# Kernel tuning notes

Hardware: AMD Instinct MI355X
Metric: run time of the kernel (lower is better)

## Reference

```python
import jax, jax.numpy as jnp
import numpy as np

EPS = 1e-6

def setup_inputs() -> dict:
    key = jax.random.key(0)
    ks = jax.random.split(key, 6)
    N, E, Din, H, D = 50000, 800000, 256, 4, 32
    x = jax.random.normal(ks[0], (N, Din), dtype=jnp.float32)
    adj_indices = jax.random.randint(ks[1], (E, 2), 0, N, dtype=jnp.int32)
    adj_weights = jax.random.uniform(ks[2], (E,), dtype=jnp.float32)
    W = jax.random.normal(ks[3], (Din, H * D), dtype=jnp.float32) * (1.0 / np.sqrt(Din))
    a_src = jax.random.normal(ks[4], (H, D), dtype=jnp.float32)
    a_dst = jax.random.normal(ks[5], (H, D), dtype=jnp.float32)
    return {"x": x, "adj_indices": adj_indices, "adj_weights": adj_weights,
            "W": W, "a_src": a_src, "a_dst": a_dst}

def reference(x, adj_indices, adj_weights, W, a_src, a_dst):
    N = x.shape[0]
    H, D = a_src.shape
    h = (x @ W).reshape(N, H, D)                       # [N,H,D]
    src = adj_indices[:, 0]
    dst = adj_indices[:, 1]
    hs = h[src]                                        # [E,H,D]
    hd = h[dst]                                        # [E,H,D]
    raw = jnp.einsum('ehd,hd->eh', hs, a_src) + jnp.einsum('ehd,hd->eh', hd, a_dst)
    gate = jnp.clip(adj_weights, EPS, None)[:, None]   # [E,1]
    scores = jnp.tanh(raw) + jnp.log(gate)             # [E,H]
    # per-destination segment softmax (numerically stable)
    seg_max = jax.ops.segment_max(scores, dst, num_segments=N)   # [N,H]
    ex = jnp.exp(scores - seg_max[dst])
    denom = jax.ops.segment_sum(ex, dst, num_segments=N)         # [N,H]
    alpha = ex / denom[dst]                            # softmax over edges per dst
    alpha = alpha * gate
    messages = alpha[:, :, None] * hs                  # [E,H,D]
    out = jax.ops.segment_sum(messages, dst, num_segments=N)     # [N,H,D]
    out = out.reshape(N, H * D)
    return jax.nn.gelu(out, approximate=False)
```

## Files before the change

### kernel.cpp

```cpp
#include <hip/hip_runtime.h>
#include <hip/hip_bf16.h>

#define N_NODES 50000
#define N_EDGES 800000
#define DIN 256
#define HD 128
#define NH 4
#define CAP 64
#define CSTR 16

#define GROWS 64
#define LDKH 136

#define GEMM_BLOCKS ((N_NODES + GROWS - 1) / GROWS)
#define SCAT_BLOCKS ((N_EDGES + 255) / 256)

typedef __bf16 bf16x8 __attribute__((ext_vector_type(8)));
typedef float  f32x4  __attribute__((ext_vector_type(4)));

static __device__ __forceinline__ unsigned short f2bu(float v) {
  union { __hip_bfloat16 b; unsigned short u; } c;
  c.b = __float2bfloat16(v);
  return c.u;
}

static __device__ __forceinline__ unsigned short f2hu(float v) {
  union { _Float16 h; unsigned short u; } c;
  c.h = (_Float16)v;
  return c.u;
}

static __device__ __forceinline__ float hu2f(unsigned short u) {
  union { _Float16 h; unsigned short u; } c;
  c.u = u;
  return (float)c.h;
}

__global__ void init_kernel(const float* __restrict__ W,
                            unsigned short* __restrict__ Wt,
                            int* __restrict__ cursor) {
  int i = blockIdx.x * 256 + threadIdx.x;
  if (i < HD * DIN) {
    int c = i >> 8, k = i & 255;
    Wt[c * 256 + k] = f2bu(W[k * HD + c]);
  }
  if (i < N_NODES * CSTR) cursor[i] = 0;
}

__global__ __launch_bounds__(256, 4) void fused_gemm_scatter(
    const float* __restrict__ x,
    const unsigned short* __restrict__ Wt,
    const float* __restrict__ a_src,
    const float* __restrict__ a_dst,
    unsigned short* __restrict__ hbf,
    float* __restrict__ ssrc,
    float* __restrict__ sdst,
    const int2* __restrict__ adj,
    const float* __restrict__ wts,
    int* __restrict__ cursor,
    unsigned int* __restrict__ slots) {
  __shared__ unsigned short xs[GROWS * LDKH];
  const int tid = threadIdx.x;

  if (blockIdx.x >= GEMM_BLOCKS) {
    int e = (blockIdx.x - GEMM_BLOCKS) * 256 + tid;
    if (e >= N_EDGES) return;
    int2 sd = adj[e];
    if ((unsigned)sd.x >= (unsigned)N_NODES || (unsigned)sd.y >= (unsigned)N_NODES) return;
    float g = fmaxf(wts[e], 1e-6f);
    int pos = atomicAdd(&cursor[sd.y * CSTR], 1);
    if (pos >= CAP) pos = CAP - 1;
    unsigned packed = ((unsigned)f2hu(g) << 16) | (unsigned)sd.x;
    __builtin_nontemporal_store(packed, &slots[((size_t)sd.y << 6) + pos]);
    return;
  }

  const int row0 = blockIdx.x * GROWS;
  const int wid  = tid >> 6;
  const int lane = tid & 63;
  const int m    = lane & 15;
  const int q    = lane >> 4;

  f32x4 acc[8];
#pragma unroll
  for (int t = 0; t < 8; t++) acc[t] = (f32x4){0.f, 0.f, 0.f, 0.f};

#pragma unroll
  for (int ks = 0; ks < 2; ks++) {
#pragma unroll
    for (int it = 0; it < 8; it++) {
      int i  = it * 256 + tid;
      int r  = i >> 5;
      int kq = i & 31;
      int row = row0 + r;
      float4 v = make_float4(0.f, 0.f, 0.f, 0.f);
      if (row < N_NODES) v = *(const float4*)(x + (size_t)row * DIN + ks * 128 + 4 * kq);
      ushort4 b;
      b.x = f2bu(v.x); b.y = f2bu(v.y); b.z = f2bu(v.z); b.w = f2bu(v.w);
      *(ushort4*)&xs[r * LDKH + 4 * kq] = b;
    }
    __syncthreads();

    const unsigned short* xbase = &xs[(wid * 16 + m) * LDKH];
#pragma unroll
    for (int s = 0; s < 4; s++) {
      bf16x8 afrag = *(const bf16x8*)(xbase + 32 * s + 8 * q);
#pragma unroll
      for (int t = 0; t < 8; t++) {
        bf16x8 bfrag = *(const bf16x8*)(Wt + (size_t)(16 * t + m) * 256 + ks * 128 + 32 * s + 8 * q);
        acc[t] = __builtin_amdgcn_mfma_f32_16x16x32_bf16(afrag, bfrag, acc[t], 0, 0, 0);
      }
    }
    __syncthreads();
  }

#pragma unroll
  for (int t = 0; t < 8; t++) {
#pragma unroll
    for (int r = 0; r < 4; r++) {
      int row = row0 + wid * 16 + q * 4 + r;
      if (row < N_NODES) hbf[(size_t)row * HD + 16 * t + m] = f2bu(acc[t][r]);
    }
  }

  float as[8], ad[8];
#pragma unroll
  for (int t = 0; t < 8; t++) {
    as[t] = a_src[16 * t + m];
    ad[t] = a_dst[16 * t + m];
  }
#pragma unroll
  for (int r = 0; r < 4; r++) {
    float ps[NH] = {0.f, 0.f, 0.f, 0.f};
    float pd[NH] = {0.f, 0.f, 0.f, 0.f};
#pragma unroll
    for (int t = 0; t < 8; t++) {
      ps[t >> 1] = fmaf(acc[t][r], as[t], ps[t >> 1]);
      pd[t >> 1] = fmaf(acc[t][r], ad[t], pd[t >> 1]);
    }
#pragma unroll
    for (int mm = 8; mm >= 1; mm >>= 1) {
#pragma unroll
      for (int hh = 0; hh < NH; hh++) {
        ps[hh] += __shfl_xor(ps[hh], mm, 64);
        pd[hh] += __shfl_xor(pd[hh], mm, 64);
      }
    }
    int row = row0 + wid * 16 + q * 4 + r;
    if (m == 0 && row < N_NODES) {
#pragma unroll
      for (int hh = 0; hh < NH; hh++) {
        ssrc[row * NH + hh] = ps[hh];
        sdst[row * NH + hh] = pd[hh];
      }
    }
  }
}

__global__ __launch_bounds__(128, 8) void node_kernel(
    const int* __restrict__ cursor,
    const unsigned int* __restrict__ slots,
    const float4* __restrict__ ssrc4,
    const float4* __restrict__ sdst4,
    const unsigned int* __restrict__ hbf32,
    float* __restrict__ out) {
  const int tid  = threadIdx.x;
  const int wid  = tid >> 6;
  const int lane = tid & 63;
  const int n    = blockIdx.x * 2 + wid;
  const int hh   = lane >> 4;

  int deg = cursor[n * CSTR];
  if (deg > CAP) deg = CAP;

  __shared__ int    sidx[2][CAP];
  __shared__ float4 swv[2][CAP];

  float4 ex = make_float4(0.f, 0.f, 0.f, 0.f);
  if (lane < deg) {
    unsigned sl = slots[((size_t)n << 6) + lane];
    int s = (int)(sl & 0xffffu);
    float g = hu2f((unsigned short)(sl >> 16));
    float4 ss = ssrc4[s];
    float4 sd = sdst4[n];
    ex.x = g * expf(tanhf(ss.x + sd.x));
    ex.y = g * expf(tanhf(ss.y + sd.y));
    ex.z = g * expf(tanhf(ss.z + sd.z));
    ex.w = g * expf(tanhf(ss.w + sd.w));
    sidx[wid][lane] = s;
    swv[wid][lane] = make_float4(ex.x * g, ex.y * g, ex.z * g, ex.w * g);
  }

  float4 tot = ex;
#pragma unroll
  for (int mm = 32; mm >= 1; mm >>= 1) {
    tot.x += __shfl_xor(tot.x, mm, 64);
    tot.y += __shfl_xor(tot.y, mm, 64);
    tot.z += __shfl_xor(tot.z, mm, 64);
    tot.w += __shfl_xor(tot.w, mm, 64);
  }
  float dn  = (hh == 0) ? tot.x : (hh == 1) ? tot.y : (hh == 2) ? tot.z : tot.w;
  float inv = (dn > 0.f) ? 1.f / dn : 0.f;
  __syncthreads();

  float acc0 = 0.f, acc1 = 0.f;
  int j = 0;
  for (; j + 4 <= deg; j += 4) {
    int s0 = sidx[wid][j + 0], s1 = sidx[wid][j + 1];
    int s2 = sidx[wid][j + 2], s3 = sidx[wid][j + 3];
    unsigned u0 = hbf32[(size_t)s0 * (HD / 2) + lane];
    unsigned u1 = hbf32[(size_t)s1 * (HD / 2) + lane];
    unsigned u2 = hbf32[(size_t)s2 * (HD / 2) + lane];
    unsigned u3 = hbf32[(size_t)s3 * (HD / 2) + lane];
    float w0 = ((const float*)&swv[wid][j + 0])[hh];
    float w1 = ((const float*)&swv[wid][j + 1])[hh];
    float w2 = ((const float*)&swv[wid][j + 2])[hh];
    float w3 = ((const float*)&swv[wid][j + 3])[hh];
    acc0 = fmaf(w0, __uint_as_float(u0 << 16), acc0);
    acc1 = fmaf(w0, __uint_as_float(u0 & 0xffff0000u), acc1);
    acc0 = fmaf(w1, __uint_as_float(u1 << 16), acc0);
    acc1 = fmaf(w1, __uint_as_float(u1 & 0xffff0000u), acc1);
    acc0 = fmaf(w2, __uint_as_float(u2 << 16), acc0);
    acc1 = fmaf(w2, __uint_as_float(u2 & 0xffff0000u), acc1);
    acc0 = fmaf(w3, __uint_as_float(u3 << 16), acc0);
    acc1 = fmaf(w3, __uint_as_float(u3 & 0xffff0000u), acc1);
  }
  for (; j < deg; j++) {
    int s0 = sidx[wid][j];
    unsigned u0 = hbf32[(size_t)s0 * (HD / 2) + lane];
    float w0 = ((const float*)&swv[wid][j])[hh];
    acc0 = fmaf(w0, __uint_as_float(u0 << 16), acc0);
    acc1 = fmaf(w0, __uint_as_float(u0 & 0xffff0000u), acc1);
  }
  acc0 *= inv;
  acc1 *= inv;

  float2 gl;
  gl.x = 0.5f * acc0 * (1.f + erff(acc0 * 0.70710678118654752f));
  gl.y = 0.5f * acc1 * (1.f + erff(acc1 * 0.70710678118654752f));
  *(float2*)&out[(size_t)n * HD + 2 * lane] = gl;
}

extern "C" void kernel_launch(void* const* d_in, const int* in_sizes, int n_in,
                              void* d_out, int out_size, void* d_ws, size_t ws_size,
                              hipStream_t stream) {
  const float* x     = (const float*)d_in[0];
  const int2*  adj   = (const int2*)d_in[1];
  const float* wts   = (const float*)d_in[2];
  const float* W     = (const float*)d_in[3];
  const float* a_src = (const float*)d_in[4];
  const float* a_dst = (const float*)d_in[5];
  float* out = (float*)d_out;

  char* p = (char*)d_ws;
  auto carve = [&](size_t bytes) {
    char* q = p;
    p += (bytes + 255) & ~(size_t)255;
    return (void*)q;
  };
  unsigned short* hbf = (unsigned short*)carve((size_t)N_NODES * HD * sizeof(unsigned short));
  unsigned short* Wt  = (unsigned short*)carve((size_t)HD * DIN * sizeof(unsigned short));
  float* ssrc   = (float*)carve((size_t)N_NODES * NH * sizeof(float));
  float* sdst   = (float*)carve((size_t)N_NODES * NH * sizeof(float));
  unsigned int* slots = (unsigned int*)carve((size_t)N_NODES * CAP * sizeof(unsigned int));
  int*   cursor = (int*)carve((size_t)N_NODES * CSTR * sizeof(int));

  init_kernel<<<(N_NODES * CSTR + 255) / 256, 256, 0, stream>>>(W, Wt, cursor);
  fused_gemm_scatter<<<GEMM_BLOCKS + SCAT_BLOCKS, 256, 0, stream>>>(
      x, Wt, a_src, a_dst, hbf, ssrc, sdst, adj, wts, cursor, slots);
  node_kernel<<<N_NODES / 2, 128, 0, stream>>>(cursor, slots, (const float4*)ssrc,
                                               (const float4*)sdst,
                                               (const unsigned int*)hbf, out);
}
```

Baseline: 192.6 us.

## Prefetch second K-half of x, pre-swizzle W fragments, unroll gather loop by eight

The GEMM stage now loads the second 128-column half of x into registers while the MFMAs for the first half run, so global latency overlaps with compute. W is pre-permuted in the init kernel into MFMA fragment order, making each B-fragment load one contiguous 16-byte read per lane. The node kernel's gather loop is unrolled from 4 to 8 edges to keep more independent loads in flight, and the launch bounds are relaxed on both kernels. The cost is higher register use, which may lower occupancy. The source index is also masked to 16 bits, which truncates node IDs above 65535 even though N is 50000.

```diff
diff --git a/kernel.cpp b/kernel.cpp
--- a/kernel.cpp
+++ b/kernel.cpp
@@ -37,19 +37,26 @@
 }
 
 __global__ void init_kernel(const float* __restrict__ W,
-                            unsigned short* __restrict__ Wt,
+                            unsigned short* __restrict__ WtF,
                             int* __restrict__ cursor) {
   int i = blockIdx.x * 256 + threadIdx.x;
   if (i < HD * DIN) {
-    int c = i >> 8, k = i & 255;
-    Wt[c * 256 + k] = f2bu(W[k * HD + c]);
+    int j    = i & 7;
+    int lane = (i >> 3) & 63;
+    int t    = (i >> 9) & 7;
+    int s    = (i >> 12) & 3;
+    int ks   = (i >> 14) & 1;
+    int m = lane & 15, q = lane >> 4;
+    int k = ks * 128 + 32 * s + 8 * q + j;
+    int c = 16 * t + m;
+    WtF[i] = f2bu(W[k * HD + c]);
   }
   if (i < N_NODES * CSTR) cursor[i] = 0;
 }
 
-__global__ __launch_bounds__(256, 4) void fused_gemm_scatter(
+__global__ void fused_gemm_scatter(
     const float* __restrict__ x,
-    const unsigned short* __restrict__ Wt,
+    const unsigned short* __restrict__ WtF,
     const float* __restrict__ a_src,
     const float* __restrict__ a_dst,
     unsigned short* __restrict__ hbf,
@@ -70,7 +77,7 @@
     float g = fmaxf(wts[e], 1e-6f);
     int pos = atomicAdd(&cursor[sd.y * CSTR], 1);
     if (pos >= CAP) pos = CAP - 1;
-    unsigned packed = ((unsigned)f2hu(g) << 16) | (unsigned)sd.x;
+    unsigned packed = ((unsigned)f2hu(g) << 16) | (unsigned)(sd.x & 0xffff);
     __builtin_nontemporal_store(packed, &slots[((size_t)sd.y << 6) + pos]);
     return;
   }
@@ -81,37 +88,76 @@
   const int m    = lane & 15;
   const int q    = lane >> 4;
 
+  float4 v0[8];
+#pragma unroll
+  for (int it = 0; it < 8; it++) {
+    int i = it * 256 + tid, r = i >> 5, kq = i & 31;
+    int row = row0 + r;
+    v0[it] = (row < N_NODES) ? *(const float4*)(x + (size_t)row * DIN + 4 * kq)
+                             : make_float4(0.f, 0.f, 0.f, 0.f);
+  }
+#pragma unroll
+  for (int it = 0; it < 8; it++) {
+    int i = it * 256 + tid, r = i >> 5, kq = i & 31;
+    ushort4 b;
+    b.x = f2bu(v0[it].x); b.y = f2bu(v0[it].y); b.z = f2bu(v0[it].z); b.w = f2bu(v0[it].w);
+    *(ushort4*)&xs[r * LDKH + 4 * kq] = b;
+  }
+  __syncthreads();
+
   f32x4 acc[8];
 #pragma unroll
   for (int t = 0; t < 8; t++) acc[t] = (f32x4){0.f, 0.f, 0.f, 0.f};
 
-#pragma unroll
-  for (int ks = 0; ks < 2; ks++) {
-#pragma unroll
-    for (int it = 0; it < 8; it++) {
-      int i  = it * 256 + tid;
-      int r  = i >> 5;
-      int kq = i & 31;
-      int row = row0 + r;
-      float4 v = make_float4(0.f, 0.f, 0.f, 0.f);
-      if (row < N_NODES) v = *(const float4*)(x + (size_t)row * DIN + ks * 128 + 4 * kq);
-      ushort4 b;
-      b.x = f2bu(v.x); b.y = f2bu(v.y); b.z = f2bu(v.z); b.w = f2bu(v.w);
-      *(ushort4*)&xs[r * LDKH + 4 * kq] = b;
-    }
-    __syncthreads();
-
-    const unsigned short* xbase = &xs[(wid * 16 + m) * LDKH];
-#pragma unroll
-    for (int s = 0; s < 4; s++) {
-      bf16x8 afrag = *(const bf16x8*)(xbase + 32 * s + 8 * q);
-#pragma unroll
-      for (int t = 0; t < 8; t++) {
-        bf16x8 bfrag = *(const bf16x8*)(Wt + (size_t)(16 * t + m) * 256 + ks * 128 + 32 * s + 8 * q);
-        acc[t] = __builtin_amdgcn_mfma_f32_16x16x32_bf16(afrag, bfrag, acc[t], 0, 0, 0);
-      }
-    }
-    __syncthreads();
+  const unsigned short* xbase = &xs[(wid * 16 + m) * LDKH];
+
+  bf16x8 a0[4];
+#pragma unroll
+  for (int s = 0; s < 4; s++) a0[s] = *(const bf16x8*)(xbase + 32 * s + 8 * q);
+
+  float4 v1[8];
+#pragma unroll
+  for (int it = 0; it < 8; it++) {
+    int i = it * 256 + tid, r = i >> 5, kq = i & 31;
+    int row = row0 + r;
+    v1[it] = (row < N_NODES) ? *(const float4*)(x + (size_t)row * DIN + 128 + 4 * kq)
+                             : make_float4(0.f, 0.f, 0.f, 0.f);
+  }
+
+#pragma unroll
+  for (int s = 0; s < 4; s++) {
+    bf16x8 bfr[8];
+#pragma unroll
+    for (int t = 0; t < 8; t++)
+      bfr[t] = *(const bf16x8*)(WtF + (size_t)((0 * 4 + s) * 8 + t) * 512 + lane * 8);
+#pragma unroll
+    for (int t = 0; t < 8; t++)
+      acc[t] = __builtin_amdgcn_mfma_f32_16x16x32_bf16(a0[s], bfr[t], acc[t], 0, 0, 0);
+  }
+  __syncthreads();
+
+#pragma unroll
+  for (int it = 0; it < 8; it++) {
+    int i = it * 256 + tid, r = i >> 5, kq = i & 31;
+    ushort4 b;
+    b.x = f2bu(v1[it].x); b.y = f2bu(v1[it].y); b.z = f2bu(v1[it].z); b.w = f2bu(v1[it].w);
+    *(ushort4*)&xs[r * LDKH + 4 * kq] = b;
+  }
+  __syncthreads();
+
+  bf16x8 a1[4];
+#pragma unroll
+  for (int s = 0; s < 4; s++) a1[s] = *(const bf16x8*)(xbase + 32 * s + 8 * q);
+
+#pragma unroll
+  for (int s = 0; s < 4; s++) {
+    bf16x8 bfr[8];
+#pragma unroll
+    for (int t = 0; t < 8; t++)
+      bfr[t] = *(const bf16x8*)(WtF + (size_t)((1 * 4 + s) * 8 + t) * 512 + lane * 8);
+#pragma unroll
+    for (int t = 0; t < 8; t++)
+      acc[t] = __builtin_amdgcn_mfma_f32_16x16x32_bf16(a1[s], bfr[t], acc[t], 0, 0, 0);
   }
 
 #pragma unroll
@@ -157,7 +203,7 @@
   }
 }
 
-__global__ __launch_bounds__(128, 8) void node_kernel(
+__global__ __launch_bounds__(128, 4) void node_kernel(
     const int* __restrict__ cursor,
     const unsigned int* __restrict__ slots,
     const float4* __restrict__ ssrc4,
@@ -205,17 +251,27 @@
 
   float acc0 = 0.f, acc1 = 0.f;
   int j = 0;
-  for (; j + 4 <= deg; j += 4) {
+  for (; j + 8 <= deg; j += 8) {
     int s0 = sidx[wid][j + 0], s1 = sidx[wid][j + 1];
     int s2 = sidx[wid][j + 2], s3 = sidx[wid][j + 3];
+    int s4 = sidx[wid][j + 4], s5 = sidx[wid][j + 5];
+    int s6 = sidx[wid][j + 6], s7 = sidx[wid][j + 7];
     unsigned u0 = hbf32[(size_t)s0 * (HD / 2) + lane];
     unsigned u1 = hbf32[(size_t)s1 * (HD / 2) + lane];
     unsigned u2 = hbf32[(size_t)s2 * (HD / 2) + lane];
     unsigned u3 = hbf32[(size_t)s3 * (HD / 2) + lane];
+    unsigned u4 = hbf32[(size_t)s4 * (HD / 2) + lane];
+    unsigned u5 = hbf32[(size_t)s5 * (HD / 2) + lane];
+    unsigned u6 = hbf32[(size_t)s6 * (HD / 2) + lane];
+    unsigned u7 = hbf32[(size_t)s7 * (HD / 2) + lane];
     float w0 = ((const float*)&swv[wid][j + 0])[hh];
     float w1 = ((const float*)&swv[wid][j + 1])[hh];
     float w2 = ((const float*)&swv[wid][j + 2])[hh];
     float w3 = ((const float*)&swv[wid][j + 3])[hh];
+    float w4 = ((const float*)&swv[wid][j + 4])[hh];
+    float w5 = ((const float*)&swv[wid][j + 5])[hh];
+    float w6 = ((const float*)&swv[wid][j + 6])[hh];
+    float w7 = ((const float*)&swv[wid][j + 7])[hh];
     acc0 = fmaf(w0, __uint_as_float(u0 << 16), acc0);
     acc1 = fmaf(w0, __uint_as_float(u0 & 0xffff0000u), acc1);
     acc0 = fmaf(w1, __uint_as_float(u1 << 16), acc0);
@@ -224,6 +280,14 @@
     acc1 = fmaf(w2, __uint_as_float(u2 & 0xffff0000u), acc1);
     acc0 = fmaf(w3, __uint_as_float(u3 << 16), acc0);
     acc1 = fmaf(w3, __uint_as_float(u3 & 0xffff0000u), acc1);
+    acc0 = fmaf(w4, __uint_as_float(u4 << 16), acc0);
+    acc1 = fmaf(w4, __uint_as_float(u4 & 0xffff0000u), acc1);
+    acc0 = fmaf(w5, __uint_as_float(u5 << 16), acc0);
+    acc1 = fmaf(w5, __uint_as_float(u5 & 0xffff0000u), acc1);
+    acc0 = fmaf(w6, __uint_as_float(u6 << 16), acc0);
+    acc1 = fmaf(w6, __uint_as_float(u6 & 0xffff0000u), acc1);
+    acc0 = fmaf(w7, __uint_as_float(u7 << 16), acc0);
+    acc1 = fmaf(w7, __uint_as_float(u7 & 0xffff0000u), acc1);
   }
   for (; j < deg; j++) {
     int s0 = sidx[wid][j];
@@ -259,15 +323,15 @@
     return (void*)q;
   };
   unsigned short* hbf = (unsigned short*)carve((size_t)N_NODES * HD * sizeof(unsigned short));
-  unsigned short* Wt  = (unsigned short*)carve((size_t)HD * DIN * sizeof(unsigned short));
+  unsigned short* WtF = (unsigned short*)carve((size_t)HD * DIN * sizeof(unsigned short));
   float* ssrc   = (float*)carve((size_t)N_NODES * NH * sizeof(float));
   float* sdst   = (float*)carve((size_t)N_NODES * NH * sizeof(float));
   unsigned int* slots = (unsigned int*)carve((size_t)N_NODES * CAP * sizeof(unsigned int));
   int*   cursor = (int*)carve((size_t)N_NODES * CSTR * sizeof(int));
 
-  init_kernel<<<(N_NODES * CSTR + 255) / 256, 256, 0, stream>>>(W, Wt, cursor);
+  init_kernel<<<(N_NODES * CSTR + 255) / 256, 256, 0, stream>>>(W, WtF, cursor);
   fused_gemm_scatter<<<GEMM_BLOCKS + SCAT_BLOCKS, 256, 0, stream>>>(
-      x, Wt, a_src, a_dst, hbf, ssrc, sdst, adj, wts, cursor, slots);
+      x, WtF, a_src, a_dst, hbf, ssrc, sdst, adj, wts, cursor, slots);
   node_kernel<<<N_NODES / 2, 128, 0, stream>>>(cursor, slots, (const float4*)ssrc,
                                                (const float4*)sdst,
                                                (const unsigned int*)hbf, out);
```

After: 192.3 us. Within noise of the previous version (-0.2%).
